# Performance work log

Measured on AMD Instinct MI355X. Metric: run time of the kernel, lower is better.

The kernel has to match this reference:

```python
import jax, jax.numpy as jnp
import numpy as np

N = 50000
E = 800000
IN_DIM = 16
H = 128
L = 4
EDGE_DIM = 7
LN_EPS = 1e-5


def _linear_params(key, fan_in, fan_out):
    kw, kb = jax.random.split(key)
    w = jax.random.normal(kw, (fan_in, fan_out), jnp.float32) * 0.02
    b = jax.random.normal(kb, (fan_out,), jnp.float32) * 0.02
    return w, b


def setup_inputs() -> dict:
    key = jax.random.key(0)
    ks = jax.random.split(key, 20)
    x = jax.random.normal(ks[0], (N, IN_DIM), jnp.float32)
    pos = jax.random.uniform(ks[1], (N, 3), jnp.float32) * 10.0
    row = jax.random.randint(ks[2], (E,), 0, N, jnp.int32)
    # guarantee no self-loops so distance > 0 (radius_graph uses loop=False)
    off = jax.random.randint(ks[3], (E,), 1, N, jnp.int32)
    col = (row + off) % N
    edge_index = jnp.stack([row, col], axis=0)

    W_in, b_in = _linear_params(ks[4], IN_DIM, H)

    def stack_layers(kbase, fan_in, fan_out):
        ws, bs = [], []
        for l in range(L):
            w, b = _linear_params(jax.random.fold_in(kbase, l), fan_in, fan_out)
            ws.append(w); bs.append(b)
        return jnp.stack(ws), jnp.stack(bs)

    We1, be1 = stack_layers(ks[5], 2 * H + EDGE_DIM, H)
    We2, be2 = stack_layers(ks[6], H, H)
    We3, be3 = stack_layers(ks[7], H, H)
    Wn1, bn1 = stack_layers(ks[8], H + H, H)
    Wn2, bn2 = stack_layers(ks[9], H, H)
    Wn3, bn3 = stack_layers(ks[10], H, H)
    ln_g = jnp.ones((L, H), jnp.float32)
    ln_b = jnp.zeros((L, H), jnp.float32)

    return {
        'x': x, 'pos': pos, 'edge_index': edge_index,
        'W_in': W_in, 'b_in': b_in,
        'We1': We1, 'be1': be1, 'We2': We2, 'be2': be2, 'We3': We3, 'be3': be3,
        'Wn1': Wn1, 'bn1': bn1, 'Wn2': Wn2, 'bn2': bn2, 'Wn3': Wn3, 'bn3': bn3,
        'ln_g': ln_g, 'ln_b': ln_b,
    }


def reference(x, pos, edge_index, W_in, b_in, We1, be1, We2, be2, We3, be3,
              Wn1, bn1, Wn2, bn2, Wn3, bn3, ln_g, ln_b):
    n = x.shape[0]
    row, col = edge_index[0], edge_index[1]  # row=source, col=target (PyG)
    rel_pos = pos[col] - pos[row]                       # (E, 3)
    dist = jnp.linalg.norm(rel_pos, axis=1, keepdims=True)  # (E, 1)
    edge_attr = jnp.concatenate([rel_pos, dist], axis=1)    # (E, 4)

    h = x @ W_in + b_in  # (N, H)
    num_layers = We1.shape[0]
    for l in range(num_layers):
        mom = h[:, 3:6]
        rel_mom = mom[col] - mom[row]                        # (E, 3)
        ea = jnp.concatenate([edge_attr, rel_mom], axis=1)   # (E, 7)
        # PyG: x_i = x[target=col], x_j = x[source=row]; EdgeMLP concats [h_i, h_j, ea]
        m = jnp.concatenate([h[col], h[row], ea], axis=1)    # (E, 2H+7)
        m = jax.nn.relu(m @ We1[l] + be1[l])
        m = jax.nn.relu(m @ We2[l] + be2[l])
        m = m @ We3[l] + be3[l]                              # (E, H)
        agg = jax.ops.segment_sum(m, col, num_segments=n)    # scatter-add to targets
        u = jnp.concatenate([h, agg], axis=1)                # (N, 2H)
        u = jax.nn.relu(u @ Wn1[l] + bn1[l])
        u = jax.nn.relu(u @ Wn2[l] + bn2[l])
        u = u @ Wn3[l] + bn3[l]                              # (N, H)
        h = h + u
        mean = jnp.mean(h, axis=-1, keepdims=True)
        var = jnp.mean(jnp.square(h - mean), axis=-1, keepdims=True)
        h = (h - mean) * jax.lax.rsqrt(var + LN_EPS) * ln_g[l] + ln_b[l]
    return h
```

## Files before the change

kernel.cpp:

```cpp
#include <hip/hip_runtime.h>
#include <stdint.h>

#define NN 50000
#define NE 800000
#define HD 128
#define NL 4
#define NM 64
#define EB 128
#define SCH ((NN + 1023) / 1024)

typedef __bf16 bf16x8 __attribute__((ext_vector_type(8)));
typedef __bf16 bf16x4 __attribute__((ext_vector_type(4)));
typedef float  f32x4  __attribute__((ext_vector_type(4)));

__device__ __forceinline__ f32x4 mfma16(bf16x8 a, bf16x8 b, f32x4 c) {
  return __builtin_amdgcn_mfma_f32_16x16x32_bf16(a, b, c, 0, 0, 0);
}

template<int MT, int NT>
__device__ __forceinline__ void zero_acc(f32x4 (&acc)[MT][NT]) {
#pragma unroll
  for (int i = 0; i < MT; ++i)
#pragma unroll
    for (int j = 0; j < NT; ++j) acc[i][j] = f32x4{0.f, 0.f, 0.f, 0.f};
}

template<int MT, int NT, int KS>
__device__ __forceinline__ void gemm_chunk(const __bf16* A, int sa,
    const __bf16* __restrict__ Bt, int Krow, int k0,
    int m_off, int n_off, int lane, f32x4 (&acc)[MT][NT])
{
  const int arow = lane & 15;
  const int quad = lane >> 4;
  bf16x8 b[KS][NT];
#pragma unroll
  for (int ks = 0; ks < KS; ++ks)
#pragma unroll
    for (int nt = 0; nt < NT; ++nt)
      b[ks][nt] = *reinterpret_cast<const bf16x8*>(
          Bt + (size_t)(n_off + nt * 16 + arow) * Krow + k0 + ks * 32 + quad * 8);
#pragma unroll
  for (int ks = 0; ks < KS; ++ks) {
    const int k = k0 + ks * 32 + quad * 8;
    bf16x8 a[MT];
#pragma unroll
    for (int mt = 0; mt < MT; ++mt)
      a[mt] = *reinterpret_cast<const bf16x8*>(A + (m_off + mt * 16 + arow) * sa + k);
#pragma unroll
    for (int mt = 0; mt < MT; ++mt)
#pragma unroll
      for (int nt = 0; nt < NT; ++nt)
        acc[mt][nt] = mfma16(a[mt], b[ks][nt], acc[mt][nt]);
  }
}

template<int MT, int NT, bool RELU>
__device__ __forceinline__ void store_tile(__bf16* O, int so,
    const float* __restrict__ bias, int m_off, int n_off, int lane,
    f32x4 (&acc)[MT][NT])
{
  const int quad = lane >> 4;
  const int cl = lane & 15;
#pragma unroll
  for (int nt = 0; nt < NT; ++nt) {
    const int col = n_off + nt * 16 + cl;
    const float bv = bias[col];
#pragma unroll
    for (int mt = 0; mt < MT; ++mt)
#pragma unroll
      for (int r = 0; r < 4; ++r) {
        const int row = m_off + mt * 16 + quad * 4 + r;
        float v = acc[mt][nt][r] + bv;
        if (RELU) v = fmaxf(v, 0.f);
        O[row * so + col] = (__bf16)v;
      }
  }
}

__global__ void prep_w(const float* __restrict__ W, __bf16* __restrict__ Wt,
                       int K0, int Kp) {
  int idx = blockIdx.x * 256 + threadIdx.x;
  int total = NL * HD * Kp;
  if (idx >= total) return;
  int l = idx / (HD * Kp);
  int rem = idx - l * HD * Kp;
  int n = rem / Kp;
  int k = rem - n * Kp;
  float v = (k < K0) ? W[((size_t)l * K0 + k) * HD + n] : 0.f;
  Wt[idx] = (__bf16)v;
}

__global__ void prep_pqw(const float* __restrict__ We1,
                         __bf16* __restrict__ Wtopt, __bf16* __restrict__ Wbott) {
  int idx = blockIdx.x * 256 + threadIdx.x;
  if (idx >= NL * HD * HD) return;
  int l = idx / (HD * HD);
  int rem = idx - l * HD * HD;
  int n = rem >> 7;
  int k = rem & 127;
  const float* W = We1 + (size_t)l * 263 * HD;
  float extra = (k >= 3 && k < 6) ? W[(260 + k - 3) * HD + n] : 0.f;
  Wtopt[idx] = (__bf16)(W[k * HD + n] + extra);
  Wbott[idx] = (__bf16)(W[(128 + k) * HD + n] - extra);
}

__global__ void h0_kernel(const float* __restrict__ x, const float* __restrict__ W,
                          const float* __restrict__ b, float* __restrict__ H32,
                          __bf16* __restrict__ HB) {
  int idx = blockIdx.x * 256 + threadIdx.x;
  if (idx >= NN * HD) return;
  int node = idx >> 7, j = idx & 127;
  const float* xr = x + node * 16;
  float s = b[j];
#pragma unroll
  for (int k = 0; k < 16; ++k) s += xr[k] * W[k * HD + j];
  H32[idx] = s;
  HB[idx] = (__bf16)s;
}

__global__ void hist_kernel(const int* __restrict__ ei, int* __restrict__ cnt) {
  int e = blockIdx.x * 256 + threadIdx.x;
  if (e < NE) atomicAdd(&cnt[ei[NE + e]], 1);
}

__global__ void scan_kernel(const int* __restrict__ cnt, int* __restrict__ cur) {
  __shared__ int wsum[16];
  const int t = threadIdx.x;
  const int lane = t & 63, wid = t >> 6;
  const int base = t * SCH;
  int s = 0;
  for (int k = 0; k < SCH; ++k) {
    int i = base + k;
    if (i < NN) s += cnt[i];
  }
  int incl = s;
#pragma unroll
  for (int off = 1; off < 64; off <<= 1) {
    int u = __shfl_up(incl, off, 64);
    if (lane >= off) incl += u;
  }
  if (lane == 63) wsum[wid] = incl;
  __syncthreads();
  int woff = 0;
  for (int k = 0; k < wid; ++k) woff += wsum[k];
  int run = woff + incl - s;
  for (int k = 0; k < SCH; ++k) {
    int i = base + k;
    if (i < NN) { cur[i] = run; run += cnt[i]; }
  }
}

__global__ void scatter_kernel(const int* __restrict__ ei, int* __restrict__ cur,
                               int* __restrict__ ROWS, int* __restrict__ COLS) {
  int e = blockIdx.x * 256 + threadIdx.x;
  if (e < NE) {
    int r = ei[e], c = ei[NE + e];
    int p = atomicAdd(&cur[c], 1);
    ROWS[p] = r;
    COLS[p] = c;
  }
}

__global__ void dist_kernel(const float* __restrict__ pos,
                            const int* __restrict__ ROWS, const int* __restrict__ COLS,
                            __bf16* __restrict__ DSTb) {
  int p = blockIdx.x * 256 + threadIdx.x;
  if (p >= NE) return;
  int r = ROWS[p], c = COLS[p];
  float dx = pos[c * 3 + 0] - pos[r * 3 + 0];
  float dy = pos[c * 3 + 1] - pos[r * 3 + 1];
  float dz = pos[c * 3 + 2] - pos[r * 3 + 2];
  DSTb[p] = (__bf16)sqrtf(dx * dx + dy * dy + dz * dz);
}

__global__ __launch_bounds__(256, 4) void pq_kernel(
    const __bf16* __restrict__ HB, const float* __restrict__ pos,
    const __bf16* __restrict__ Wtopt, const __bf16* __restrict__ Wbott,
    const float* __restrict__ W4xyz,
    const float* __restrict__ be1,
    __bf16* __restrict__ PB, __bf16* __restrict__ QB)
{
  const int task = blockIdx.x * 4 + (threadIdx.x >> 6);
  const int lane = threadIdx.x & 63;
  const int g = task & 1;
  const int base = (task >> 1) * 32;
  if (base >= NN) return;
  const int arow = lane & 15, quad = lane >> 4, cl = lane & 15;

  const __bf16* Wt = g ? Wbott : Wtopt;
  __bf16* O = g ? QB : PB;
  f32x4 acc[2][8];
  zero_acc(acc);
#pragma unroll
  for (int ks = 0; ks < 4; ++ks) {
    const int k = ks * 32 + quad * 8;
    bf16x8 b[8];
#pragma unroll
    for (int nt = 0; nt < 8; ++nt)
      b[nt] = *reinterpret_cast<const bf16x8*>(Wt + (size_t)(nt * 16 + arow) * HD + k);
    bf16x8 a[2];
#pragma unroll
    for (int mt = 0; mt < 2; ++mt) {
      int row = base + mt * 16 + arow;
      if (row >= NN) row = NN - 1;
      a[mt] = *reinterpret_cast<const bf16x8*>(HB + (size_t)row * HD + k);
    }
#pragma unroll
    for (int mt = 0; mt < 2; ++mt)
#pragma unroll
      for (int nt = 0; nt < 8; ++nt)
        acc[mt][nt] = mfma16(a[mt], b[nt], acc[mt][nt]);
  }
  float px[2][4], py[2][4], pz[2][4];
#pragma unroll
  for (int mt = 0; mt < 2; ++mt)
#pragma unroll
    for (int r = 0; r < 4; ++r) {
      int row = base + mt * 16 + quad * 4 + r;
      if (row >= NN) row = NN - 1;
      px[mt][r] = pos[row * 3 + 0];
      py[mt][r] = pos[row * 3 + 1];
      pz[mt][r] = pos[row * 3 + 2];
    }
#pragma unroll
  for (int nt = 0; nt < 8; ++nt) {
    const int col = nt * 16 + cl;
    const float w0 = W4xyz[col], w1 = W4xyz[HD + col], w2 = W4xyz[2 * HD + col];
    const float bb = g ? 0.f : be1[col];
#pragma unroll
    for (int mt = 0; mt < 2; ++mt)
#pragma unroll
      for (int r = 0; r < 4; ++r) {
        const int row = base + mt * 16 + quad * 4 + r;
        if (row < NN) {
          float dot = px[mt][r] * w0 + py[mt][r] * w1 + pz[mt][r] * w2;
          float v = acc[mt][nt][r] + (g ? -dot : dot) + bb;
          O[(size_t)row * HD + col] = (__bf16)v;
        }
      }
  }
}

__global__ __launch_bounds__(512, 4) void edge_kernel(
    const __bf16* __restrict__ PB, const __bf16* __restrict__ QB,
    const __bf16* __restrict__ DSTb,
    const int* __restrict__ ROWS, const int* __restrict__ COLS,
    const float* __restrict__ w4d,
    const __bf16* __restrict__ We2t, const __bf16* __restrict__ We3t,
    const float* __restrict__ be2, const float* __restrict__ be3,
    float* __restrict__ AGG)
{
  __shared__ __bf16 S1[EB * 136];
  __shared__ __bf16 S2[EB * 136];
  __shared__ float w4ds[HD], be2s[HD], be3s[HD];
  __shared__ int colS[EB];
  __shared__ unsigned long long bmaskS[EB / 64];
  const int t = threadIdx.x;

  const int nwg = gridDim.x;
  const int q = nwg >> 3, r8 = nwg & 7;
  const int xcd = blockIdx.x & 7, idx8 = blockIdx.x >> 3;
  const int bswz = (xcd < r8 ? xcd * (q + 1) : r8 * (q + 1) + (xcd - r8) * q) + idx8;
  const int base = bswz * EB;

  if (t < HD) { w4ds[t] = w4d[t]; be2s[t] = be2[t]; be3s[t] = be3[t]; }
  if (t < EB) colS[t] = COLS[base + t];
  __syncthreads();

  if (t < EB) {
    int d = (t == EB - 1) || (colS[t + 1] != colS[t]);
    unsigned long long bm = __ballot(d);
    if ((t & 63) == 0) bmaskS[t >> 6] = bm;
  }

  {
    const int i = t >> 2, cg = t & 3;
    const int p = base + i;
    const int c = colS[i];
    const int r = ROWS[p];
    const float dist = (float)DSTb[p];
    const __bf16* Prow = PB + (size_t)c * HD;
    const __bf16* Qrow = QB + (size_t)r * HD;
#pragma unroll
    for (int u = 0; u < 4; ++u) {
      const int ch = cg * 4 + u;
      bf16x8 pv = *reinterpret_cast<const bf16x8*>(Prow + ch * 8);
      bf16x8 qv = *reinterpret_cast<const bf16x8*>(Qrow + ch * 8);
      bf16x8 o;
#pragma unroll
      for (int j = 0; j < 8; ++j) {
        const int col = ch * 8 + j;
        float f = (float)pv[j] + (float)qv[j] + dist * w4ds[col];
        o[j] = (__bf16)fmaxf(f, 0.f);
      }
      *reinterpret_cast<bf16x8*>(S1 + i * 136 + ch * 8) = o;
    }
  }
  __syncthreads();

  const int w = t >> 6, lane = t & 63;
  const int m_off = (w >> 2) * 64, n_off = (w & 3) * 32;
  const int arow = lane & 15, quad = lane >> 4, cl = lane & 15;

  f32x4 acc[4][2];
#pragma unroll
  for (int g = 0; g < 2; ++g) {
    const __bf16* Wt = g ? We3t : We2t;
    const float* bs = g ? be3s : be2s;
    const __bf16* Sin  = g ? S2 : S1;
    __bf16* Sout = g ? S1 : S2;

    bf16x8 b[4][2];
#pragma unroll
    for (int ks = 0; ks < 4; ++ks)
#pragma unroll
      for (int nt = 0; nt < 2; ++nt)
        b[ks][nt] = *reinterpret_cast<const bf16x8*>(
            Wt + (size_t)(n_off + nt * 16 + arow) * HD + ks * 32 + quad * 8);

    zero_acc(acc);
#pragma unroll
    for (int ks = 0; ks < 4; ++ks) {
      const int k = ks * 32 + quad * 8;
      bf16x8 a[4];
#pragma unroll
      for (int mt = 0; mt < 4; ++mt)
        a[mt] = *reinterpret_cast<const bf16x8*>(Sin + (m_off + mt * 16 + arow) * 136 + k);
#pragma unroll
      for (int mt = 0; mt < 4; ++mt)
#pragma unroll
        for (int nt = 0; nt < 2; ++nt)
          acc[mt][nt] = mfma16(a[mt], b[ks][nt], acc[mt][nt]);
    }
#pragma unroll
    for (int nt = 0; nt < 2; ++nt) {
      const int col = n_off + nt * 16 + cl;
      const float bv = bs[col];
#pragma unroll
      for (int mt = 0; mt < 4; ++mt)
#pragma unroll
        for (int r = 0; r < 4; ++r) {
          const int row = m_off + mt * 16 + quad * 4 + r;
          float v = acc[mt][nt][r] + bv;
          if (!g) v = fmaxf(v, 0.f);
          Sout[row * 136 + col] = (__bf16)v;
        }
    }
    __syncthreads();
  }

  if (t < HD) {
    const int j = t;
    const unsigned long long m0 = bmaskS[0];
    const unsigned long long m1 = bmaskS[1] | (1ull << 63);
    float s = 0.f;
    bool first = true;
#pragma unroll 8
    for (int i = 0; i < EB; ++i) {
      s += (float)S1[i * 136 + j];
      const bool b = (i < 64) ? ((m0 >> i) & 1ull) : ((m1 >> (i - 64)) & 1ull);
      if (b) {
        float* a = &AGG[(size_t)colS[i] * HD + j];
        if (first || i == EB - 1) atomicAdd(a, s);
        else *a = s;
        first = false;
        s = 0.f;
      }
    }
  }
}

__global__ __launch_bounds__(256, 4) void node_kernel(
    const __bf16* __restrict__ HBin, float* __restrict__ AGG,
    const __bf16* __restrict__ Wn1t, const __bf16* __restrict__ Wn2t,
    const __bf16* __restrict__ Wn3t,
    const float* __restrict__ bn1, const float* __restrict__ bn2,
    const float* __restrict__ bn3,
    const float* __restrict__ lng, const float* __restrict__ lnb,
    float* __restrict__ H32, __bf16* __restrict__ HBout,
    float* __restrict__ dout)
{
  __shared__ float SB[NM * 136];
  __shared__ float ps[NM][2], psq[NM][2];
  __shared__ float mean_s[NM], rstd_s[NM];
  __bf16* B16 = reinterpret_cast<__bf16*>(SB);
  const int t = threadIdx.x;
  const int base = blockIdx.x * NM;

  {
    const int i0 = t >> 4, s = t & 15;
#pragma unroll
    for (int g = 0; g < NM / 16; ++g) {
      const int i = g * 16 + i0;
      const int node = base + i;
      uint4 v = make_uint4(0, 0, 0, 0);
      if (node < NN) v = *(reinterpret_cast<const uint4*>(HBin + (size_t)node * HD) + s);
      *reinterpret_cast<uint4*>(&B16[i * 264 + s * 8]) = v;
    }
  }
  for (int idx = t; idx < NM * 32; idx += 256) {
    const int i = idx >> 5, c4 = idx & 31;
    const int node = base + i;
    float4 v = make_float4(0.f, 0.f, 0.f, 0.f);
    if (node < NN) {
      float4* ap = reinterpret_cast<float4*>(AGG + (size_t)node * HD + c4 * 4);
      v = *ap;
      *ap = make_float4(0.f, 0.f, 0.f, 0.f);
    }
    __bf16* d = &B16[i * 264 + HD + c4 * 4];
    d[0] = (__bf16)v.x; d[1] = (__bf16)v.y; d[2] = (__bf16)v.z; d[3] = (__bf16)v.w;
  }
  __syncthreads();

  const int w = t >> 6, lane = t & 63;
  const int m_off = (w >> 1) * 32, n_off = (w & 1) * 64;
  f32x4 acc[2][4];
  __bf16* reg0 = B16;
  __bf16* reg1 = B16 + NM * 136;

  zero_acc(acc);
  gemm_chunk<2, 4, 4>(B16, 264, Wn1t, 256, 0,   m_off, n_off, lane, acc);
  gemm_chunk<2, 4, 4>(B16, 264, Wn1t, 256, 128, m_off, n_off, lane, acc);
  __syncthreads();
  store_tile<2, 4, true>(reg0, 136, bn1, m_off, n_off, lane, acc);
  __syncthreads();
  zero_acc(acc);
  gemm_chunk<2, 4, 4>(reg0, 136, Wn2t, 128, 0, m_off, n_off, lane, acc);
  store_tile<2, 4, true>(reg1, 136, bn2, m_off, n_off, lane, acc);
  __syncthreads();
  zero_acc(acc);
  gemm_chunk<2, 4, 4>(reg1, 136, Wn3t, 128, 0, m_off, n_off, lane, acc);
  __syncthreads();

  {
    const int quad = lane >> 4, cl = lane & 15;
#pragma unroll
    for (int nt = 0; nt < 4; ++nt) {
      const int col = n_off + nt * 16 + cl;
      const float bv = bn3[col];
#pragma unroll
      for (int mt = 0; mt < 2; ++mt)
#pragma unroll
        for (int r = 0; r < 4; ++r) {
          const int row = m_off + mt * 16 + quad * 4 + r;
          const int node = base + row;
          float hv = (node < NN) ? H32[(size_t)node * HD + col] : 0.f;
          SB[row * 136 + col] = hv + acc[mt][nt][r] + bv;
        }
    }
  }
  __syncthreads();
  if (t < 128) {
    const int r = t >> 1, hh = t & 1;
    float s = 0.f, sq = 0.f;
    for (int j = hh * 64; j < hh * 64 + 64; ++j) {
      float v = SB[r * 136 + j];
      s += v; sq += v * v;
    }
    ps[r][hh] = s; psq[r][hh] = sq;
  }
  __syncthreads();
  if (t < NM) {
    float s = ps[t][0] + ps[t][1];
    float sq = psq[t][0] + psq[t][1];
    float mean = s * (1.f / HD);
    float var = sq * (1.f / HD) - mean * mean;
    mean_s[t] = mean;
    rstd_s[t] = rsqrtf(var + 1e-5f);
  }
  __syncthreads();
  for (int idx = t; idx < NM * HD; idx += 256) {
    const int r = idx >> 7, j = idx & 127;
    const int node = base + r;
    if (node < NN) {
      float v = (SB[r * 136 + j] - mean_s[r]) * rstd_s[r] * lng[j] + lnb[j];
      H32[(size_t)node * HD + j] = v;
      HBout[(size_t)node * HD + j] = (__bf16)v;
      if (dout) dout[(size_t)node * HD + j] = v;
    }
  }
}

extern "C" void kernel_launch(void* const* d_in, const int* in_sizes, int n_in,
                              void* d_out, int out_size, void* d_ws, size_t ws_size,
                              hipStream_t stream)
{
  const float* x    = (const float*)d_in[0];
  const float* pos  = (const float*)d_in[1];
  const int*   ei   = (const int*)d_in[2];
  const float* W_in = (const float*)d_in[3];
  const float* b_in = (const float*)d_in[4];
  const float* We1  = (const float*)d_in[5];
  const float* be1  = (const float*)d_in[6];
  const float* We2  = (const float*)d_in[7];
  const float* be2  = (const float*)d_in[8];
  const float* We3  = (const float*)d_in[9];
  const float* be3  = (const float*)d_in[10];
  const float* Wn1  = (const float*)d_in[11];
  const float* bn1  = (const float*)d_in[12];
  const float* Wn2  = (const float*)d_in[13];
  const float* bn2  = (const float*)d_in[14];
  const float* Wn3  = (const float*)d_in[15];
  const float* bn3  = (const float*)d_in[16];
  const float* lng  = (const float*)d_in[17];
  const float* lnb  = (const float*)d_in[18];
  float* out = (float*)d_out;

  char* ws = (char*)d_ws;
  size_t off = 0;
  auto alloc = [&](size_t bytes) -> char* {
    char* p = ws + off;
    off += (bytes + 255) & ~(size_t)255;
    return p;
  };
  __bf16* Wtopt = (__bf16*)alloc((size_t)NL * HD * HD * 2);
  __bf16* Wbott = (__bf16*)alloc((size_t)NL * HD * HD * 2);
  __bf16* We2t = (__bf16*)alloc((size_t)NL * HD * HD * 2);
  __bf16* We3t = (__bf16*)alloc((size_t)NL * HD * HD * 2);
  __bf16* Wn1t = (__bf16*)alloc((size_t)NL * HD * 256 * 2);
  __bf16* Wn2t = (__bf16*)alloc((size_t)NL * HD * HD * 2);
  __bf16* Wn3t = (__bf16*)alloc((size_t)NL * HD * HD * 2);
  __bf16* DSTb = (__bf16*)alloc((size_t)NE * 2);
  float*  H32  = (float*) alloc((size_t)NN * HD * 4);
  __bf16* HB   = (__bf16*)alloc((size_t)NN * HD * 2);
  __bf16* PB   = (__bf16*)alloc((size_t)NN * HD * 2);
  __bf16* QB   = (__bf16*)alloc((size_t)NN * HD * 2);
  float*  AGG  = (float*) alloc((size_t)NN * HD * 4);
  int*    CNT  = (int*)   alloc((size_t)NN * 4);
  int*    CUR  = (int*)   alloc((size_t)NN * 4);
  int*    ROWS = (int*)   alloc((size_t)NE * 4);
  int*    COLS = (int*)   alloc((size_t)NE * 4);

  hipMemsetAsync(CNT, 0, (size_t)NN * 4, stream);
  hipMemsetAsync(AGG, 0, (size_t)NN * HD * 4, stream);
  prep_pqw<<<(NL * HD * HD + 255) / 256, 256, 0, stream>>>(We1, Wtopt, Wbott);
  prep_w<<<(NL * HD * HD + 255) / 256, 256, 0, stream>>>(We2, We2t, 128, 128);
  prep_w<<<(NL * HD * HD + 255) / 256, 256, 0, stream>>>(We3, We3t, 128, 128);
  prep_w<<<(NL * HD * 256 + 255) / 256, 256, 0, stream>>>(Wn1, Wn1t, 256, 256);
  prep_w<<<(NL * HD * HD + 255) / 256, 256, 0, stream>>>(Wn2, Wn2t, 128, 128);
  prep_w<<<(NL * HD * HD + 255) / 256, 256, 0, stream>>>(Wn3, Wn3t, 128, 128);
  h0_kernel<<<(NN * HD + 255) / 256, 256, 0, stream>>>(x, W_in, b_in, H32, HB);
  hist_kernel<<<(NE + 255) / 256, 256, 0, stream>>>(ei, CNT);
  scan_kernel<<<1, 1024, 0, stream>>>(CNT, CUR);
  scatter_kernel<<<(NE + 255) / 256, 256, 0, stream>>>(ei, CUR, ROWS, COLS);
  dist_kernel<<<(NE + 255) / 256, 256, 0, stream>>>(pos, ROWS, COLS, DSTb);

  const int pq_tasks = 2 * ((NN + 31) / 32);
  const int pq_blocks = (pq_tasks + 3) / 4;
  for (int l = 0; l < NL; ++l) {
    const float* We1l = We1 + (size_t)l * 263 * HD;
    pq_kernel<<<pq_blocks, 256, 0, stream>>>(HB, pos,
        Wtopt + (size_t)l * HD * HD, Wbott + (size_t)l * HD * HD,
        We1l + 256 * HD,
        be1 + l * HD, PB, QB);
    edge_kernel<<<NE / EB, 512, 0, stream>>>(PB, QB, DSTb, ROWS, COLS,
        We1l + 259 * HD,
        We2t + (size_t)l * HD * HD, We3t + (size_t)l * HD * HD,
        be2 + l * HD, be3 + l * HD, AGG);
    node_kernel<<<(NN + NM - 1) / NM, 256, 0, stream>>>(HB, AGG,
        Wn1t + (size_t)l * HD * 256, Wn2t + (size_t)l * HD * HD,
        Wn3t + (size_t)l * HD * HD,
        bn1 + l * HD, bn2 + l * HD, bn3 + l * HD,
        lng + l * HD, lnb + l * HD,
        H32, HB, (l == NL - 1) ? out : nullptr);
  }
}
```

Before: 1.414 ms.

## Fuse distance computation into CSR scatter and split segment reduction across all threads

```diff
diff --git a/kernel.cpp b/kernel.cpp
--- a/kernel.cpp
+++ b/kernel.cpp
@@ -151,26 +151,20 @@
 }
 
 __global__ void scatter_kernel(const int* __restrict__ ei, int* __restrict__ cur,
-                               int* __restrict__ ROWS, int* __restrict__ COLS) {
+                               const float* __restrict__ pos,
+                               int* __restrict__ ROWS, int* __restrict__ COLS,
+                               __bf16* __restrict__ DSTb) {
   int e = blockIdx.x * 256 + threadIdx.x;
   if (e < NE) {
     int r = ei[e], c = ei[NE + e];
     int p = atomicAdd(&cur[c], 1);
     ROWS[p] = r;
     COLS[p] = c;
-  }
-}
-
-__global__ void dist_kernel(const float* __restrict__ pos,
-                            const int* __restrict__ ROWS, const int* __restrict__ COLS,
-                            __bf16* __restrict__ DSTb) {
-  int p = blockIdx.x * 256 + threadIdx.x;
-  if (p >= NE) return;
-  int r = ROWS[p], c = COLS[p];
-  float dx = pos[c * 3 + 0] - pos[r * 3 + 0];
-  float dy = pos[c * 3 + 1] - pos[r * 3 + 1];
-  float dz = pos[c * 3 + 2] - pos[r * 3 + 2];
-  DSTb[p] = (__bf16)sqrtf(dx * dx + dy * dy + dz * dz);
+    float dx = pos[c * 3 + 0] - pos[r * 3 + 0];
+    float dy = pos[c * 3 + 1] - pos[r * 3 + 1];
+    float dz = pos[c * 3 + 2] - pos[r * 3 + 2];
+    DSTb[p] = (__bf16)sqrtf(dx * dx + dy * dy + dz * dz);
+  }
 }
 
 __global__ __launch_bounds__(256, 4) void pq_kernel(
@@ -349,21 +343,17 @@
     __syncthreads();
   }
 
-  if (t < HD) {
-    const int j = t;
-    const unsigned long long m0 = bmaskS[0];
-    const unsigned long long m1 = bmaskS[1] | (1ull << 63);
+  {
+    const int j = t & 127, qtr = t >> 7;
+    const int i0 = qtr * 32;
+    unsigned int m = (unsigned int)(bmaskS[qtr >> 1] >> ((qtr & 1) * 32));
+    m |= 0x80000000u;
     float s = 0.f;
-    bool first = true;
-#pragma unroll 8
-    for (int i = 0; i < EB; ++i) {
+    for (int r = 0; r < 32; ++r) {
+      const int i = i0 + r;
       s += (float)S1[i * 136 + j];
-      const bool b = (i < 64) ? ((m0 >> i) & 1ull) : ((m1 >> (i - 64)) & 1ull);
-      if (b) {
-        float* a = &AGG[(size_t)colS[i] * HD + j];
-        if (first || i == EB - 1) atomicAdd(a, s);
-        else *a = s;
-        first = false;
+      if ((m >> r) & 1u) {
+        atomicAdd(&AGG[(size_t)colS[i] * HD + j], s);
         s = 0.f;
       }
     }
@@ -542,8 +532,7 @@
   h0_kernel<<<(NN * HD + 255) / 256, 256, 0, stream>>>(x, W_in, b_in, H32, HB);
   hist_kernel<<<(NE + 255) / 256, 256, 0, stream>>>(ei, CNT);
   scan_kernel<<<1, 1024, 0, stream>>>(CNT, CUR);
-  scatter_kernel<<<(NE + 255) / 256, 256, 0, stream>>>(ei, CUR, ROWS, COLS);
-  dist_kernel<<<(NE + 255) / 256, 256, 0, stream>>>(pos, ROWS, COLS, DSTb);
+  scatter_kernel<<<(NE + 255) / 256, 256, 0, stream>>>(ei, CUR, pos, ROWS, COLS, DSTb);
 
   const int pq_tasks = 2 * ((NN + 31) / 32);
   const int pq_blocks = (pq_tasks + 3) / 4;
```

Result: faster. 1.282 ms (-9.4%).
